# Optimization experiments

Measured on AMD Instinct MI355X. Metric: run time of the kernel, lower is better.

## Reference

```python
import jax, jax.numpy as jnp
import numpy as np

NUM_HEADS = 16
HEAD_DIM = 64  # 1024 / 16


def setup_inputs() -> dict:
    key = jax.random.key(0)
    ks = jax.random.split(key, 8)
    B, S, D = 2, 2048, 1024
    s = 0.02
    return {
        "hidden_states_q": jax.random.normal(ks[0], (B, S, D), jnp.float32),
        "hidden_states_k": jax.random.normal(ks[1], (B, S, D), jnp.float32),
        "hidden_states_v": jax.random.normal(ks[2], (B, S, D), jnp.float32),
        "Wq": jax.random.normal(ks[3], (D, D), jnp.float32) * s,
        "bq": jnp.zeros((D,), jnp.float32),
        "Wk": jax.random.normal(ks[4], (D, D), jnp.float32) * s,
        "bk": jnp.zeros((D,), jnp.float32),
        "Wv": jax.random.normal(ks[5], (D, D), jnp.float32) * s,
        "bv": jnp.zeros((D,), jnp.float32),
        "Wp": jax.random.normal(ks[6], (D, D), jnp.float32) * s,
        "bp": jnp.zeros((D,), jnp.float32),
    }


def _split_heads(x):
    B, S, D = x.shape
    return x.reshape(B, S, NUM_HEADS, HEAD_DIM).transpose(0, 2, 1, 3)  # [B,H,S,dh]


def reference(hidden_states_q, hidden_states_k, hidden_states_v,
              Wq, bq, Wk, bk, Wv, bv, Wp, bp):
    # Projections (Linear / Conv1D are both x @ W + b in this parameterization)
    q = _split_heads(hidden_states_q @ Wq + bq)
    k = _split_heads(hidden_states_k @ Wk + bk)
    v = _split_heads(hidden_states_v @ Wv + bv)
    scale = 1.0 / jnp.sqrt(jnp.asarray(HEAD_DIM, q.dtype))
    # NOTE: no causal mask is applied in the original _attn (mask asserted None)
    attn = jnp.einsum("bhqd,bhkd->bhqk", q, k) * scale
    attn = jax.nn.softmax(attn, axis=-1)  # attn_dropout is identity in eval
    out = jnp.einsum("bhqk,bhkd->bhqd", attn, v)
    B, H, S, dh = out.shape
    out = out.transpose(0, 2, 1, 3).reshape(B, S, H * dh)
    out = out @ Wp + bp  # resid_dropout identity in eval
    return out
```

## Files before the change

### kernel.cpp

```cpp
#include <hip/hip_runtime.h>
#include <stdint.h>


typedef _Float16 f16;
typedef __attribute__((ext_vector_type(8))) _Float16 f16x8;
typedef __attribute__((ext_vector_type(4))) _Float16 f16x4;
typedef __attribute__((ext_vector_type(2))) _Float16 f16x2;
typedef __attribute__((ext_vector_type(4))) float f32x4;
typedef __attribute__((ext_vector_type(16))) float f32x16;
typedef __attribute__((ext_vector_type(2))) unsigned u32x2;

#define NB 2
#define SEQ 2048
#define DMODEL 1024
#define NH 16
#define DH 64

#define QSCALE 0.1803368801111601f

__device__ __forceinline__ void gload_lds16(const void* g, void* l) {
  __builtin_amdgcn_global_load_lds(
      (const __attribute__((address_space(1))) unsigned int*)g,
      (__attribute__((address_space(3))) unsigned int*)l, 16, 0, 0);
}

__device__ __forceinline__ void plswap(unsigned& a, unsigned& b) {
  u32x2 r = __builtin_amdgcn_permlane32_swap(a, b, false, false);
  a = r[0];
  b = r[1];
}

__global__ __launch_bounds__(256) void prep(
    const float* __restrict__ hq, const float* __restrict__ hk,
    const float* __restrict__ hv, f16* __restrict__ xq, f16* __restrict__ xk,
    f16* __restrict__ xv, const float* __restrict__ w0,
    const float* __restrict__ w1, const float* __restrict__ w2,
    const float* __restrict__ w3, f16* __restrict__ t0, f16* __restrict__ t1,
    f16* __restrict__ t2, f16* __restrict__ t3) {
  __shared__ float tile[64][65];
  const int z = blockIdx.z;
  if (z < 3) {
    const float* src = z == 0 ? hq : (z == 1 ? hk : hv);
    f16* dst = z == 0 ? xq : (z == 1 ? xk : xv);
    int i = (blockIdx.x * 256 + threadIdx.x) * 8;
    float4 a = *(const float4*)(src + i);
    float4 b = *(const float4*)(src + i + 4);
    f16x8 o;
    o[0] = (f16)a.x; o[1] = (f16)a.y; o[2] = (f16)a.z; o[3] = (f16)a.w;
    o[4] = (f16)b.x; o[5] = (f16)b.y; o[6] = (f16)b.z; o[7] = (f16)b.w;
    *(f16x8*)(dst + i) = o;
    return;
  }
  if (blockIdx.x >= 256) return;
  const float* W; f16* T;
  switch (z - 3) {
    case 0: W = w0; T = t0; break;
    case 1: W = w1; T = t1; break;
    case 2: W = w2; T = t2; break;
    default: W = w3; T = t3; break;
  }
  int r0 = (blockIdx.x >> 4) * 64, c0 = (blockIdx.x & 15) * 64;
  for (int it = 0; it < 16; ++it) {
    int idx = it * 256 + threadIdx.x;
    int r = idx >> 6, c = idx & 63;
    tile[r][c] = W[(size_t)(r0 + r) * DMODEL + c0 + c];
  }
  __syncthreads();
  for (int it = 0; it < 16; ++it) {
    int idx = it * 256 + threadIdx.x;
    int r = idx >> 6, c = idx & 63;
    T[(size_t)(c0 + r) * DMODEL + r0 + c] = (f16)tile[c][r];
  }
}

__global__ __launch_bounds__(256) void gemm128(
    const f16* __restrict__ xq, const f16* __restrict__ xk,
    const f16* __restrict__ xv,
    const f16* __restrict__ wqt, const f16* __restrict__ wkt,
    const f16* __restrict__ wvt,
    const float* __restrict__ bq, const float* __restrict__ bk,
    const float* __restrict__ bv,
    f16* __restrict__ qo, f16* __restrict__ ko, f16* __restrict__ vto) {
  __shared__ char lds[32768];
  char* ldsA = lds;
  char* ldsB = lds + 16384;

  const int bid = blockIdx.x;
  const int mode = bid >> 8;
  const int lin = bid & 255;
  const int m0 = ((lin & 7) + 8 * ((lin >> 3) & 3)) * 128;
  const int n0 = (lin >> 5) * 128;

  const f16* Am; const f16* Bt; const float* bias; float oscale = 1.0f;
  if (mode == 0)      { Am = xq; Bt = wqt; bias = bq; oscale = QSCALE; }
  else if (mode == 1) { Am = xk; Bt = wkt; bias = bk; }
  else                { Am = xv; Bt = wvt; bias = bv; }

  const int tid = threadIdx.x;
  const int l = tid & 63, w = tid >> 6;
  const int g = l >> 4, c = l & 15;
  const int wr = w >> 1, wc = w & 1;

  const int srow = w * 8 + (l >> 3);
  const int schunk = (l & 7) ^ ((l >> 3) & 7);

  f32x4 acc[4][4] = {};

  for (int k0 = 0; k0 < DMODEL; k0 += 64) {
#pragma unroll
    for (int it = 0; it < 4; ++it) {
      int row = it * 32 + srow;
      gload_lds16(Am + (size_t)(m0 + row) * DMODEL + k0 + schunk * 8,
                  ldsA + it * 4096 + w * 1024);
    }
#pragma unroll
    for (int it = 0; it < 4; ++it) {
      int row = it * 32 + srow;
      gload_lds16(Bt + (size_t)(n0 + row) * DMODEL + k0 + schunk * 8,
                  ldsB + it * 4096 + w * 1024);
    }
    __syncthreads();
    f16x8 af[2][4], bf[2][4];
#pragma unroll
    for (int kc = 0; kc < 2; ++kc)
#pragma unroll
      for (int i = 0; i < 4; ++i) {
        int row = wr * 64 + i * 16 + c;
        af[kc][i] = *(const f16x8*)(ldsA + row * 128 + (((kc * 4 + g) ^ (row & 7)) << 4));
        int rowb = wc * 64 + i * 16 + c;
        bf[kc][i] = *(const f16x8*)(ldsB + rowb * 128 + (((kc * 4 + g) ^ (rowb & 7)) << 4));
      }
#pragma unroll
    for (int kc = 0; kc < 2; ++kc)
#pragma unroll
      for (int i = 0; i < 4; ++i)
#pragma unroll
        for (int j = 0; j < 4; ++j)
          acc[i][j] = __builtin_amdgcn_mfma_f32_16x16x32_f16(af[kc][i], bf[kc][j],
                                                             acc[i][j], 0, 0, 0);
    __syncthreads();
  }

#pragma unroll
  for (int i = 0; i < 4; ++i) {
#pragma unroll
    for (int j = 0; j < 4; ++j) {
      int grb = m0 + wr * 64 + i * 16 + g * 4;
      int gc = n0 + wc * 64 + j * 16 + c;
      float bval = bias[gc];
      if (mode == 2) {
        int b = grb >> 11, s = grb & 2047, h = gc >> 6, d = gc & 63;
        f16x4 pk;
#pragma unroll
        for (int e = 0; e < 4; ++e) pk[e] = (f16)(acc[i][j][e] + bval);
        *(f16x4*)(vto + ((size_t)((b * NH + h) * DH + d)) * SEQ + s) = pk;
      } else {
        f16* dst = (mode == 0) ? qo : ko;
        int b = grb >> 11, s = grb & 2047, h = gc >> 6, d = gc & 63;
#pragma unroll
        for (int e = 0; e < 4; ++e)
          dst[(((size_t)(b * NH + h) * SEQ) + (s + e)) * DH + d] =
              (f16)((acc[i][j][e] + bval) * oscale);
      }
    }
  }
}

__global__ __launch_bounds__(256) void gemm_out(
    const f16* __restrict__ ao, const f16* __restrict__ wpt,
    const float* __restrict__ bp, float* __restrict__ out) {
  __shared__ char lds[24576];
  char* ldsA = lds;
  char* ldsB = lds + 16384;

  const int lin = blockIdx.x;
  const int m0 = ((lin & 7) + 8 * ((lin >> 3) & 3)) * 128;
  const int n0 = (lin >> 5) * 64;

  const int tid = threadIdx.x;
  const int l = tid & 63, w = tid >> 6;
  const int g = l >> 4, c = l & 15;
  const int wr = w >> 1, wc = w & 1;

  const int srow = w * 8 + (l >> 3);
  const int schunk = (l & 7) ^ ((l >> 3) & 7);

  f32x4 acc[4][2] = {};

  for (int k0 = 0; k0 < DMODEL; k0 += 64) {
#pragma unroll
    for (int it = 0; it < 4; ++it) {
      int row = it * 32 + srow;
      gload_lds16(ao + (size_t)(m0 + row) * DMODEL + k0 + schunk * 8,
                  ldsA + it * 4096 + w * 1024);
    }
#pragma unroll
    for (int it = 0; it < 2; ++it) {
      int row = it * 32 + srow;
      gload_lds16(wpt + (size_t)(n0 + row) * DMODEL + k0 + schunk * 8,
                  ldsB + it * 4096 + w * 1024);
    }
    __syncthreads();
    f16x8 af[2][4], bf[2][2];
#pragma unroll
    for (int kc = 0; kc < 2; ++kc) {
#pragma unroll
      for (int i = 0; i < 4; ++i) {
        int row = wr * 64 + i * 16 + c;
        af[kc][i] = *(const f16x8*)(ldsA + row * 128 + (((kc * 4 + g) ^ (row & 7)) << 4));
      }
#pragma unroll
      for (int j = 0; j < 2; ++j) {
        int rowb = wc * 32 + j * 16 + c;
        bf[kc][j] = *(const f16x8*)(ldsB + rowb * 128 + (((kc * 4 + g) ^ (rowb & 7)) << 4));
      }
    }
#pragma unroll
    for (int kc = 0; kc < 2; ++kc)
#pragma unroll
      for (int i = 0; i < 4; ++i)
#pragma unroll
        for (int j = 0; j < 2; ++j)
          acc[i][j] = __builtin_amdgcn_mfma_f32_16x16x32_f16(af[kc][i], bf[kc][j],
                                                             acc[i][j], 0, 0, 0);
    __syncthreads();
  }

#pragma unroll
  for (int i = 0; i < 4; ++i)
#pragma unroll
    for (int j = 0; j < 2; ++j) {
      int grb = m0 + wr * 64 + i * 16 + g * 4;
      int gc = n0 + wc * 32 + j * 16 + c;
      float bval = bp[gc];
#pragma unroll
      for (int e = 0; e < 4; ++e)
        out[(size_t)(grb + e) * DMODEL + gc] = acc[i][j][e] + bval;
    }
}

__global__ __launch_bounds__(256, 2) void attn64(
    const f16* __restrict__ qg, const f16* __restrict__ kg,
    const f16* __restrict__ vtg, f16* __restrict__ aout) {
  __shared__ char lds[65536];

  const int tid = threadIdx.x;
  const int l = tid & 63, w = tid >> 6;
  const int q31 = l & 31;
  const bool hi = l >= 32;
  const int p = w & 1;
  const int qgrp = w >> 1;

  const int bid = blockIdx.x;
  const int bh = (bid & 7) + 8 * (bid >> 7);
  const int qc = (bid >> 3) & 15;
  const int q0 = qc * 128 + qgrp * 64;

  f16x8 qf0[4], qf1[4];
#pragma unroll
  for (int ks = 0; ks < 4; ++ks) {
    qf0[ks] = *(const f16x8*)(qg + ((size_t)bh * SEQ + q0 + q31) * DH + ks * 16 +
                              (hi ? 8 : 0));
    qf1[ks] = *(const f16x8*)(qg + ((size_t)bh * SEQ + q0 + 32 + q31) * DH +
                              ks * 16 + (hi ? 8 : 0));
  }

  float lsum0 = 0.0f, lsum1 = 0.0f;
  f32x16 oacc00 = {}, oacc01 = {}, oacc10 = {}, oacc11 = {};

  const int srow = w * 8 + (l >> 3);
  const int schunk = (l & 7) ^ ((l >> 3) & 7);

  auto stage = [&](int buf, int t) {
    char* baseK = lds + buf * 16384;
    char* baseV = baseK + 8192;
#pragma unroll
    for (int it = 0; it < 2; ++it) {
      int row = it * 32 + srow;
      gload_lds16(kg + ((size_t)bh * SEQ + t * 64 + row) * DH + schunk * 8,
                  baseK + it * 4096 + w * 1024);
      gload_lds16(vtg + ((size_t)bh * DH + row) * SEQ + t * 64 + schunk * 8,
                  baseV + it * 4096 + w * 1024);
    }
  };

  const f16x2 one2 = {(f16)1.0f, (f16)1.0f};

  auto softmax = [&](const f32x16& st, float& lsum, unsigned* dw) {
    float ps[16];
#pragma unroll
    for (int r = 0; r < 16; ++r) ps[r] = exp2f(st[r]);
#pragma unroll
    for (int i = 0; i < 8; ++i)
      dw[i] = __builtin_bit_cast(
          unsigned, __builtin_amdgcn_cvt_pkrtz(ps[2 * i], ps[2 * i + 1]));
    float sA = 0.0f, sB = 0.0f;
#pragma unroll
    for (int i = 0; i < 4; ++i) {
      sA = __builtin_amdgcn_fdot2(__builtin_bit_cast(f16x2, dw[i]), one2, sA, false);
      sB = __builtin_amdgcn_fdot2(__builtin_bit_cast(f16x2, dw[4 + i]), one2, sB, false);
    }
    lsum += sA + sB;
    plswap(dw[0], dw[2]);
    plswap(dw[1], dw[3]);
    plswap(dw[4], dw[6]);
    plswap(dw[5], dw[7]);
  };

  auto compute = [&](const char* ldsK) {
    const char* ldsV = ldsK + 8192;
    f32x16 st0 = {}, st1 = {};
#pragma unroll
    for (int ks = 0; ks < 4; ++ks) {
      int row = p * 32 + q31;
      int ch = ((ks * 2 + (hi ? 1 : 0)) ^ (q31 & 7)) << 4;
      f16x8 kf = *(const f16x8*)(ldsK + row * 128 + ch);
      st0 = __builtin_amdgcn_mfma_f32_32x32x16_f16(kf, qf0[ks], st0, 0, 0, 0);
      st1 = __builtin_amdgcn_mfma_f32_32x32x16_f16(kf, qf1[ks], st1, 0, 0, 0);
    }
    unsigned dw0[8], dw1[8];
    softmax(st0, lsum0, dw0);
    softmax(st1, lsum1, dw1);
#pragma unroll
    for (int ks2 = 0; ks2 < 2; ++ks2) {
      union { unsigned u[4]; f16x8 v; } pb0, pb1;
      pb0.u[0] = dw0[ks2 * 4 + 0]; pb0.u[1] = dw0[ks2 * 4 + 1];
      pb0.u[2] = dw0[ks2 * 4 + 2]; pb0.u[3] = dw0[ks2 * 4 + 3];
      pb1.u[0] = dw1[ks2 * 4 + 0]; pb1.u[1] = dw1[ks2 * 4 + 1];
      pb1.u[2] = dw1[ks2 * 4 + 2]; pb1.u[3] = dw1[ks2 * 4 + 3];
      {
        int vrow = q31;
        int ch = ((p * 4 + ks2 * 2 + (hi ? 1 : 0)) ^ (vrow & 7)) << 4;
        f16x8 vf = *(const f16x8*)(ldsV + vrow * 128 + ch);
        oacc00 = __builtin_amdgcn_mfma_f32_32x32x16_f16(vf, pb0.v, oacc00, 0, 0, 0);
        oacc10 = __builtin_amdgcn_mfma_f32_32x32x16_f16(vf, pb1.v, oacc10, 0, 0, 0);
      }
      {
        int vrow = 32 + q31;
        int ch = ((p * 4 + ks2 * 2 + (hi ? 1 : 0)) ^ (vrow & 7)) << 4;
        f16x8 vf = *(const f16x8*)(ldsV + vrow * 128 + ch);
        oacc01 = __builtin_amdgcn_mfma_f32_32x32x16_f16(vf, pb0.v, oacc01, 0, 0, 0);
        oacc11 = __builtin_amdgcn_mfma_f32_32x32x16_f16(vf, pb1.v, oacc11, 0, 0, 0);
      }
    }
  };

  stage(0, 0);
  stage(1, 1);
  stage(2, 2);

  asm volatile("s_waitcnt vmcnt(8)" ::: "memory");
  __builtin_amdgcn_s_barrier();
  __builtin_amdgcn_sched_barrier(0);
  stage(3, 3);
  compute(lds);

#pragma unroll 4
  for (int t = 1; t <= 28; ++t) {
    asm volatile("s_waitcnt vmcnt(8)" ::: "memory");
    __builtin_amdgcn_s_barrier();
    __builtin_amdgcn_sched_barrier(0);
    stage((t + 3) & 3, t + 3);
    compute(lds + (t & 3) * 16384);
  }

  asm volatile("s_waitcnt vmcnt(8)" ::: "memory");
  __builtin_amdgcn_s_barrier();
  __builtin_amdgcn_sched_barrier(0);
  compute(lds + 1 * 16384);
  asm volatile("s_waitcnt vmcnt(4)" ::: "memory");
  __builtin_amdgcn_s_barrier();
  __builtin_amdgcn_sched_barrier(0);
  compute(lds + 2 * 16384);
  asm volatile("s_waitcnt vmcnt(0)" ::: "memory");
  __builtin_amdgcn_s_barrier();
  __builtin_amdgcn_sched_barrier(0);
  compute(lds + 3 * 16384);

  __syncthreads();
  char* reg = lds + qgrp * 16896;
  if (p == 1) {
#pragma unroll
    for (int j = 0; j < 8; ++j) {
      f32x4 c0, c1;
#pragma unroll
      for (int e = 0; e < 4; ++e) {
        c0[e] = (j < 4) ? oacc00[j * 4 + e] : oacc01[(j - 4) * 4 + e];
        c1[e] = (j < 4) ? oacc10[j * 4 + e] : oacc11[(j - 4) * 4 + e];
      }
      *(f32x4*)(reg + j * 1024 + l * 16) = c0;
      *(f32x4*)(reg + 8192 + j * 1024 + l * 16) = c1;
    }
    *(float*)(reg + 16384 + l * 4) = lsum0;
    *(float*)(reg + 16640 + l * 4) = lsum1;
  }
  __syncthreads();
  if (p == 0) {
#pragma unroll
    for (int j = 0; j < 8; ++j) {
      f32x4 c0 = *(const f32x4*)(reg + j * 1024 + l * 16);
      f32x4 c1 = *(const f32x4*)(reg + 8192 + j * 1024 + l * 16);
#pragma unroll
      for (int e = 0; e < 4; ++e) {
        if (j < 4) { oacc00[j * 4 + e] += c0[e]; oacc10[j * 4 + e] += c1[e]; }
        else       { oacc01[(j - 4) * 4 + e] += c0[e]; oacc11[(j - 4) * 4 + e] += c1[e]; }
      }
    }
    float lt0 = lsum0 + *(const float*)(reg + 16384 + l * 4);
    float lt1 = lsum1 + *(const float*)(reg + 16640 + l * 4);
    lt0 += __shfl_xor(lt0, 32);
    lt1 += __shfl_xor(lt1, 32);
    float inv0 = 1.0f / lt0, inv1 = 1.0f / lt1;
    const int b = bh >> 4, h = bh & 15;
#pragma unroll
    for (int f = 0; f < 2; ++f) {
      float inv = f ? inv1 : inv0;
      int s = q0 + f * 32 + q31;
#pragma unroll
      for (int dt = 0; dt < 2; ++dt)
#pragma unroll
        for (int rg = 0; rg < 4; ++rg) {
          f16x4 pk;
#pragma unroll
          for (int j = 0; j < 4; ++j) {
            float v = f ? (dt ? oacc11[rg * 4 + j] : oacc10[rg * 4 + j])
                        : (dt ? oacc01[rg * 4 + j] : oacc00[rg * 4 + j]);
            pk[j] = (f16)(v * inv);
          }
          int d0 = dt * 32 + rg * 8 + (hi ? 4 : 0);
          *(f16x4*)(aout + ((size_t)(b * SEQ + s)) * DMODEL + h * DH + d0) = pk;
        }
    }
  }
}

extern "C" void kernel_launch(void* const* d_in, const int* in_sizes, int n_in,
                              void* d_out, int out_size, void* d_ws, size_t ws_size,
                              hipStream_t stream) {
  const float* hq = (const float*)d_in[0];
  const float* hk = (const float*)d_in[1];
  const float* hv = (const float*)d_in[2];
  const float* Wq = (const float*)d_in[3];
  const float* bq = (const float*)d_in[4];
  const float* Wk = (const float*)d_in[5];
  const float* bk = (const float*)d_in[6];
  const float* Wv = (const float*)d_in[7];
  const float* bv = (const float*)d_in[8];
  const float* Wp = (const float*)d_in[9];
  const float* bp = (const float*)d_in[10];
  float* out = (float*)d_out;

  f16* xq  = (f16*)d_ws;
  f16* xk  = xq + 4194304;
  f16* xv  = xk + 4194304;
  f16* wqt = xv + 4194304;
  f16* wkt = wqt + 1048576;
  f16* wvt = wkt + 1048576;
  f16* wpt = wvt + 1048576;
  f16* qb  = wpt + 1048576;
  f16* kb  = qb + 4194304;
  f16* vtb = kb + 4194304;
  f16* ao  = vtb + 4194304;

  prep<<<dim3(2048, 1, 7), 256, 0, stream>>>(hq, hk, hv, xq, xk, xv,
                                             Wq, Wk, Wv, Wp, wqt, wkt, wvt, wpt);
  gemm128<<<dim3(768), 256, 0, stream>>>(xq, xk, xv, wqt, wkt, wvt,
                                         bq, bk, bv, qb, kb, vtb);
  attn64<<<dim3(512), 256, 0, stream>>>(qb, kb, vtb, ao);
  gemm_out<<<dim3(512), 256, 0, stream>>>(ao, wpt, bp, out);
}
```

Baseline: 127.4 us.

## Fuse fp32-to-fp16 activation conversion into QKV GEMM and restructure attention pipeline

Removes the separate prep pass that converted the fp32 Q/K/V activations to fp16. The projection GEMM now reads fp32 activations straight from global memory into registers, converts them, and writes swizzled fp16 tiles into LDS; this saves a full write and re-read of three fp16 activation buffers. The cost is that the A-tile load is now synchronous through registers instead of a direct global-to-LDS load. The attention main loop also changes from a 4-deep staged pipeline with partial vmcnt waits to a pair-wise scheme that waits for vmcnt(0) each iteration, which may reduce load/compute overlap.

```diff
diff --git a/kernel.cpp b/kernel.cpp
--- a/kernel.cpp
+++ b/kernel.cpp
@@ -31,29 +31,13 @@
 }
 
 __global__ __launch_bounds__(256) void prep(
-    const float* __restrict__ hq, const float* __restrict__ hk,
-    const float* __restrict__ hv, f16* __restrict__ xq, f16* __restrict__ xk,
-    f16* __restrict__ xv, const float* __restrict__ w0,
-    const float* __restrict__ w1, const float* __restrict__ w2,
-    const float* __restrict__ w3, f16* __restrict__ t0, f16* __restrict__ t1,
-    f16* __restrict__ t2, f16* __restrict__ t3) {
+    const float* __restrict__ w0, const float* __restrict__ w1,
+    const float* __restrict__ w2, const float* __restrict__ w3,
+    f16* __restrict__ t0, f16* __restrict__ t1, f16* __restrict__ t2,
+    f16* __restrict__ t3) {
   __shared__ float tile[64][65];
-  const int z = blockIdx.z;
-  if (z < 3) {
-    const float* src = z == 0 ? hq : (z == 1 ? hk : hv);
-    f16* dst = z == 0 ? xq : (z == 1 ? xk : xv);
-    int i = (blockIdx.x * 256 + threadIdx.x) * 8;
-    float4 a = *(const float4*)(src + i);
-    float4 b = *(const float4*)(src + i + 4);
-    f16x8 o;
-    o[0] = (f16)a.x; o[1] = (f16)a.y; o[2] = (f16)a.z; o[3] = (f16)a.w;
-    o[4] = (f16)b.x; o[5] = (f16)b.y; o[6] = (f16)b.z; o[7] = (f16)b.w;
-    *(f16x8*)(dst + i) = o;
-    return;
-  }
-  if (blockIdx.x >= 256) return;
   const float* W; f16* T;
-  switch (z - 3) {
+  switch (blockIdx.z) {
     case 0: W = w0; T = t0; break;
     case 1: W = w1; T = t1; break;
     case 2: W = w2; T = t2; break;
@@ -74,8 +58,8 @@
 }
 
 __global__ __launch_bounds__(256) void gemm128(
-    const f16* __restrict__ xq, const f16* __restrict__ xk,
-    const f16* __restrict__ xv,
+    const float* __restrict__ hq, const float* __restrict__ hk,
+    const float* __restrict__ hv,
     const f16* __restrict__ wqt, const f16* __restrict__ wkt,
     const f16* __restrict__ wvt,
     const float* __restrict__ bq, const float* __restrict__ bk,
@@ -91,10 +75,10 @@
   const int m0 = ((lin & 7) + 8 * ((lin >> 3) & 3)) * 128;
   const int n0 = (lin >> 5) * 128;
 
-  const f16* Am; const f16* Bt; const float* bias; float oscale = 1.0f;
-  if (mode == 0)      { Am = xq; Bt = wqt; bias = bq; oscale = QSCALE; }
-  else if (mode == 1) { Am = xk; Bt = wkt; bias = bk; }
-  else                { Am = xv; Bt = wvt; bias = bv; }
+  const float* Af; const f16* Bt; const float* bias; float oscale = 1.0f;
+  if (mode == 0)      { Af = hq; Bt = wqt; bias = bq; oscale = QSCALE; }
+  else if (mode == 1) { Af = hk; Bt = wkt; bias = bk; }
+  else                { Af = hv; Bt = wvt; bias = bv; }
 
   const int tid = threadIdx.x;
   const int l = tid & 63, w = tid >> 6;
@@ -104,20 +88,32 @@
   const int srow = w * 8 + (l >> 3);
   const int schunk = (l & 7) ^ ((l >> 3) & 7);
 
+  const int arow_base = w * 4 + (l >> 4);
+  const int akb = (l & 15);
+
   f32x4 acc[4][4] = {};
 
   for (int k0 = 0; k0 < DMODEL; k0 += 64) {
-#pragma unroll
-    for (int it = 0; it < 4; ++it) {
-      int row = it * 32 + srow;
-      gload_lds16(Am + (size_t)(m0 + row) * DMODEL + k0 + schunk * 8,
-                  ldsA + it * 4096 + w * 1024);
+    f32x4 av[8];
+#pragma unroll
+    for (int rr = 0; rr < 8; ++rr) {
+      int row = rr * 16 + arow_base;
+      av[rr] = *(const f32x4*)(Af + (size_t)(m0 + row) * DMODEL + k0 + akb * 4);
     }
 #pragma unroll
     for (int it = 0; it < 4; ++it) {
       int row = it * 32 + srow;
       gload_lds16(Bt + (size_t)(n0 + row) * DMODEL + k0 + schunk * 8,
                   ldsB + it * 4096 + w * 1024);
+    }
+#pragma unroll
+    for (int rr = 0; rr < 8; ++rr) {
+      int row = rr * 16 + arow_base;
+      f16x4 h4;
+      h4[0] = (f16)av[rr][0]; h4[1] = (f16)av[rr][1];
+      h4[2] = (f16)av[rr][2]; h4[3] = (f16)av[rr][3];
+      *(f16x4*)(ldsA + row * 128 + (((akb >> 1) ^ (row & 7)) << 4) +
+                (akb & 1) * 8) = h4;
     }
     __syncthreads();
     f16x8 af[2][4], bf[2][4];
@@ -347,35 +343,19 @@
 
   stage(0, 0);
   stage(1, 1);
-  stage(2, 2);
-
-  asm volatile("s_waitcnt vmcnt(8)" ::: "memory");
-  __builtin_amdgcn_s_barrier();
-  __builtin_amdgcn_sched_barrier(0);
-  stage(3, 3);
-  compute(lds);
-
-#pragma unroll 4
-  for (int t = 1; t <= 28; ++t) {
-    asm volatile("s_waitcnt vmcnt(8)" ::: "memory");
+
+#pragma unroll 2
+  for (int tt = 0; tt < 32; tt += 2) {
+    asm volatile("s_waitcnt vmcnt(0)" ::: "memory");
     __builtin_amdgcn_s_barrier();
     __builtin_amdgcn_sched_barrier(0);
-    stage((t + 3) & 3, t + 3);
-    compute(lds + (t & 3) * 16384);
-  }
-
-  asm volatile("s_waitcnt vmcnt(8)" ::: "memory");
-  __builtin_amdgcn_s_barrier();
-  __builtin_amdgcn_sched_barrier(0);
-  compute(lds + 1 * 16384);
-  asm volatile("s_waitcnt vmcnt(4)" ::: "memory");
-  __builtin_amdgcn_s_barrier();
-  __builtin_amdgcn_sched_barrier(0);
-  compute(lds + 2 * 16384);
-  asm volatile("s_waitcnt vmcnt(0)" ::: "memory");
-  __builtin_amdgcn_s_barrier();
-  __builtin_amdgcn_sched_barrier(0);
-  compute(lds + 3 * 16384);
+    if (tt + 2 < 32) {
+      stage((tt + 2) & 3, tt + 2);
+      stage((tt + 3) & 3, tt + 3);
+    }
+    compute(lds + (tt & 3) * 16384);
+    compute(lds + ((tt + 1) & 3) * 16384);
+  }
 
   __syncthreads();
   char* reg = lds + qgrp * 16896;
@@ -450,10 +430,7 @@
   const float* bp = (const float*)d_in[10];
   float* out = (float*)d_out;
 
-  f16* xq  = (f16*)d_ws;
-  f16* xk  = xq + 4194304;
-  f16* xv  = xk + 4194304;
-  f16* wqt = xv + 4194304;
+  f16* wqt = (f16*)d_ws;
   f16* wkt = wqt + 1048576;
   f16* wvt = wkt + 1048576;
   f16* wpt = wvt + 1048576;
@@ -462,9 +439,8 @@
   f16* vtb = kb + 4194304;
   f16* ao  = vtb + 4194304;
 
-  prep<<<dim3(2048, 1, 7), 256, 0, stream>>>(hq, hk, hv, xq, xk, xv,
-                                             Wq, Wk, Wv, Wp, wqt, wkt, wvt, wpt);
-  gemm128<<<dim3(768), 256, 0, stream>>>(xq, xk, xv, wqt, wkt, wvt,
+  prep<<<dim3(256, 1, 4), 256, 0, stream>>>(Wq, Wk, Wv, Wp, wqt, wkt, wvt, wpt);
+  gemm128<<<dim3(768), 256, 0, stream>>>(hq, hk, hv, wqt, wkt, wvt,
                                          bq, bk, bv, qb, kb, vtb);
   attn64<<<dim3(512), 256, 0, stream>>>(qb, kb, vtb, ao);
   gemm_out<<<dim3(512), 256, 0, stream>>>(ao, wpt, bp, out);
```

New measurement: 135.0 us. 1.06x slower.

## Double-buffer LDS tiles in projection and output GEMMs to overlap loads

Applied to the files above, without the earlier changes.

Both the QKV projection GEMM and the output projection GEMM now use two LDS buffers. The next K-tile is issued with global_load_lds right after a single barrier, while MFMAs run on the current tile. This is meant to hide global load latency and removes one of the two barriers per iteration. In exchange the LDS footprint per block doubles (64KB and 48KB), which may reduce the number of resident blocks per CU.

```diff
diff --git a/kernel.cpp b/kernel.cpp
--- a/kernel.cpp
+++ b/kernel.cpp
@@ -81,9 +81,7 @@
     const float* __restrict__ bq, const float* __restrict__ bk,
     const float* __restrict__ bv,
     f16* __restrict__ qo, f16* __restrict__ ko, f16* __restrict__ vto) {
-  __shared__ char lds[32768];
-  char* ldsA = lds;
-  char* ldsB = lds + 16384;
+  __shared__ char lds[65536];
 
   const int bid = blockIdx.x;
   const int mode = bid >> 8;
@@ -104,22 +102,34 @@
   const int srow = w * 8 + (l >> 3);
   const int schunk = (l & 7) ^ ((l >> 3) & 7);
 
-  f32x4 acc[4][4] = {};
-
-  for (int k0 = 0; k0 < DMODEL; k0 += 64) {
+  auto stage = [&](int buf, int k0) {
+    char* base = lds + buf * 32768;
 #pragma unroll
     for (int it = 0; it < 4; ++it) {
       int row = it * 32 + srow;
       gload_lds16(Am + (size_t)(m0 + row) * DMODEL + k0 + schunk * 8,
-                  ldsA + it * 4096 + w * 1024);
+                  base + it * 4096 + w * 1024);
     }
 #pragma unroll
     for (int it = 0; it < 4; ++it) {
       int row = it * 32 + srow;
       gload_lds16(Bt + (size_t)(n0 + row) * DMODEL + k0 + schunk * 8,
-                  ldsB + it * 4096 + w * 1024);
-    }
-    __syncthreads();
+                  base + 16384 + it * 4096 + w * 1024);
+    }
+  };
+
+  f32x4 acc[4][4] = {};
+
+  stage(0, 0);
+
+  for (int kk = 0; kk < 16; ++kk) {
+    asm volatile("s_waitcnt vmcnt(0)" ::: "memory");
+    __builtin_amdgcn_s_barrier();
+    __builtin_amdgcn_sched_barrier(0);
+    if (kk + 1 < 16) stage((kk + 1) & 1, (kk + 1) * 64);
+
+    const char* ldsA = lds + (kk & 1) * 32768;
+    const char* ldsB = ldsA + 16384;
     f16x8 af[2][4], bf[2][4];
 #pragma unroll
     for (int kc = 0; kc < 2; ++kc)
@@ -138,7 +148,6 @@
         for (int j = 0; j < 4; ++j)
           acc[i][j] = __builtin_amdgcn_mfma_f32_16x16x32_f16(af[kc][i], bf[kc][j],
                                                              acc[i][j], 0, 0, 0);
-    __syncthreads();
   }
 
 #pragma unroll
@@ -169,9 +178,7 @@
 __global__ __launch_bounds__(256) void gemm_out(
     const f16* __restrict__ ao, const f16* __restrict__ wpt,
     const float* __restrict__ bp, float* __restrict__ out) {
-  __shared__ char lds[24576];
-  char* ldsA = lds;
-  char* ldsB = lds + 16384;
+  __shared__ char lds[49152];
 
   const int lin = blockIdx.x;
   const int m0 = ((lin & 7) + 8 * ((lin >> 3) & 3)) * 128;
@@ -185,22 +192,34 @@
   const int srow = w * 8 + (l >> 3);
   const int schunk = (l & 7) ^ ((l >> 3) & 7);
 
-  f32x4 acc[4][2] = {};
-
-  for (int k0 = 0; k0 < DMODEL; k0 += 64) {
+  auto stage = [&](int buf, int k0) {
+    char* base = lds + buf * 24576;
 #pragma unroll
     for (int it = 0; it < 4; ++it) {
       int row = it * 32 + srow;
       gload_lds16(ao + (size_t)(m0 + row) * DMODEL + k0 + schunk * 8,
-                  ldsA + it * 4096 + w * 1024);
+                  base + it * 4096 + w * 1024);
     }
 #pragma unroll
     for (int it = 0; it < 2; ++it) {
       int row = it * 32 + srow;
       gload_lds16(wpt + (size_t)(n0 + row) * DMODEL + k0 + schunk * 8,
-                  ldsB + it * 4096 + w * 1024);
-    }
-    __syncthreads();
+                  base + 16384 + it * 4096 + w * 1024);
+    }
+  };
+
+  f32x4 acc[4][2] = {};
+
+  stage(0, 0);
+
+  for (int kk = 0; kk < 16; ++kk) {
+    asm volatile("s_waitcnt vmcnt(0)" ::: "memory");
+    __builtin_amdgcn_s_barrier();
+    __builtin_amdgcn_sched_barrier(0);
+    if (kk + 1 < 16) stage((kk + 1) & 1, (kk + 1) * 64);
+
+    const char* ldsA = lds + (kk & 1) * 24576;
+    const char* ldsB = ldsA + 16384;
     f16x8 af[2][4], bf[2][2];
 #pragma unroll
     for (int kc = 0; kc < 2; ++kc) {
@@ -223,7 +242,6 @@
         for (int j = 0; j < 2; ++j)
           acc[i][j] = __builtin_amdgcn_mfma_f32_16x16x32_f16(af[kc][i], bf[kc][j],
                                                              acc[i][j], 0, 0, 0);
-    __syncthreads();
   }
 
 #pragma unroll
```

Measured after the change: 125.0 us. About the same (-1.9%).
